# Kernel optimization log

Measured on AMD Instinct MI355X. Metric: run time of the kernel, lower is better.

## Reference

```python
import jax, jax.numpy as jnp
import numpy as np

HEADS = 8
DIM_HEAD = 64
SCALE = DIM_HEAD ** -0.5

B, N, DIM = 4096, 16, 512  # (batch*spatial, frames, channels)
HIDDEN = HEADS * DIM_HEAD  # 512


def setup_inputs() -> dict:
    key = jax.random.key(0)
    k1, k2, k3 = jax.random.split(key, 3)
    x = jax.random.normal(k1, (B, N, DIM), dtype=jnp.float32)
    # torch Linear(dim, 3*hidden, bias=False) applied as x @ W^T; we store the
    # transposed weight directly so forward is x @ w_qkv.
    w_qkv = jax.random.normal(k2, (DIM, 3 * HIDDEN), dtype=jnp.float32) * (DIM ** -0.5)
    w_out = jax.random.normal(k3, (HIDDEN, DIM), dtype=jnp.float32) * (HIDDEN ** -0.5)
    return {"x": x, "w_qkv": w_qkv, "w_out": w_out}


def reference(x, w_qkv, w_out):
    # qkv projection and split
    qkv = x @ w_qkv                                   # [b, n, 3*hidden]
    q, k, v = jnp.split(qkv, 3, axis=-1)              # each [b, n, hidden]

    def to_heads(t):
        b, n, _ = t.shape
        return t.reshape(b, n, HEADS, DIM_HEAD).transpose(0, 2, 1, 3)  # [b, h, n, d]

    q, k, v = to_heads(q), to_heads(k), to_heads(v)

    # linear attention feature maps
    q = jax.nn.softmax(q, axis=-1) * SCALE            # softmax over d
    k = jax.nn.softmax(k, axis=-2)                    # softmax over n

    # context = k^T v : [b, h, d, e]
    context = jnp.einsum('bhnd,bhne->bhde', k, v)
    out = jnp.einsum('bhnd,bhde->bhne', q, context)   # [b, h, n, e]

    b = out.shape[0]
    out = out.transpose(0, 2, 1, 3).reshape(b, N, HIDDEN)  # [b, n, hidden]
    return out @ w_out
```

## Files before the change

kernel.cpp:

```cpp
#include <hip/hip_runtime.h>
#include <hip/hip_bf16.h>


typedef __attribute__((ext_vector_type(8))) short bf16x8;
typedef __attribute__((ext_vector_type(4))) float f32x4;

__device__ __forceinline__ unsigned short f2bf(float f) {
  __hip_bfloat16 h = __float2bfloat16(f);
  return __builtin_bit_cast(unsigned short, h);
}
__device__ __forceinline__ float bf2f(unsigned short u) {
  unsigned int v = ((unsigned int)u) << 16;
  return __builtin_bit_cast(float, v);
}
__device__ __forceinline__ void gload16(const void* g, void* l) {
  __builtin_amdgcn_global_load_lds(
      (__attribute__((address_space(1))) void*)g,
      (__attribute__((address_space(3))) void*)l, 16, 0, 0);
}

__global__ __launch_bounds__(256) void conv_x_k(const float* __restrict__ x,
                                                unsigned short* __restrict__ xb) {
  size_t i = ((size_t)blockIdx.x * 256 + threadIdx.x) * 8;
  float4 a = *(const float4*)(x + i);
  float4 b = *(const float4*)(x + i + 4);
  union { unsigned short u[8]; bf16x8 v; } o;
  o.u[0] = f2bf(a.x); o.u[1] = f2bf(a.y); o.u[2] = f2bf(a.z); o.u[3] = f2bf(a.w);
  o.u[4] = f2bf(b.x); o.u[5] = f2bf(b.y); o.u[6] = f2bf(b.z); o.u[7] = f2bf(b.w);
  *(bf16x8*)(xb + i) = o.v;
}

__global__ __launch_bounds__(256) void conv_w_k(const float* __restrict__ wq,
                                                const float* __restrict__ wo,
                                                unsigned short* __restrict__ wqt,
                                                unsigned short* __restrict__ wot) {
  int i = blockIdx.x * 256 + threadIdx.x;
  if (i < 786432) {
    int n = i >> 9, k = i & 511;
    wqt[i] = f2bf(wq[k * 1536 + n]);
  } else {
    int j = i - 786432;
    int n = j >> 9, k = j & 511;
    wot[j] = f2bf(wo[k * 512 + n]);
  }
}

#define ABUF0 0
#define ABUF1 16384
#define BBUF0 32768
#define BBUF1 49152

__device__ __forceinline__ void stage_half(const unsigned short* __restrict__ G,
                                           int grow0, unsigned short* ldsb,
                                           int tid, int kofs) {
  int r = tid >> 3;
  int c = ((tid & 7) ^ (r & 7)) << 3;
  gload16(G + (size_t)(grow0 + r) * 512 + kofs + c, ldsb + tid * 8);
  gload16(G + (size_t)(grow0 + 64 + r) * 512 + kofs + c, ldsb + 4096 + tid * 8);
}

#define RD_A(base, mh, sw)                                                   \
  _Pragma("unroll") for (int mf = 0; mf < 4; ++mf)                           \
      aF[mf] = *(const bf16x8*)&lds[(base) + (rowA + (mh)*64 + mf*16) * 64 + (sw)];
#define RD_B(base, sw)                                                       \
  _Pragma("unroll") for (int nf = 0; nf < 4; ++nf)                           \
      bF[nf] = *(const bf16x8*)&lds[(base) + (rowB + nf*16) * 64 + (sw)];
#define DO_MFMA(mh)                                                          \
  __builtin_amdgcn_s_setprio(1);                                             \
  _Pragma("unroll") for (int mf = 0; mf < 4; ++mf)                           \
  _Pragma("unroll") for (int nf = 0; nf < 4; ++nf)                           \
      acc[(mh)*4 + mf][nf] = __builtin_amdgcn_mfma_f32_16x16x32_bf16(        \
          aF[mf], bF[nf], acc[(mh)*4 + mf][nf], 0, 0, 0);                    \
  __builtin_amdgcn_s_setprio(0);
#define PBAR() __builtin_amdgcn_s_barrier()
#define LGKM0()                                          \
  do {                                                   \
    asm volatile("s_waitcnt lgkmcnt(0)" ::: "memory");   \
    __builtin_amdgcn_sched_barrier(0);                   \
  } while (0)
#define VM2() asm volatile("s_waitcnt vmcnt(2)" ::: "memory")

template <int NTN, bool OUTBF>
__global__ __launch_bounds__(512) void gemm8_k(const unsigned short* __restrict__ A,
                                               const unsigned short* __restrict__ B,
                                               void* __restrict__ Cv) {
  __shared__ __align__(16) unsigned short lds[65536];
  int orig = blockIdx.x;
  int id = (orig & 7) * (gridDim.x >> 3) + (orig >> 3);
  int mt = id / NTN, nt = id % NTN;
  int m0 = mt * 256, n0 = nt * 256;
  int tid = threadIdx.x, wid = tid >> 6, l = tid & 63;
  int wr = wid >> 2, wc = wid & 3;
  int rowA = wr * 128 + (l & 15);
  int rowB = wc * 64 + (l & 15);
  int r7 = l & 7;
  int sw0 = ((l >> 4) ^ r7) << 3;
  int sw1 = (((l >> 4) | 4) ^ r7) << 3;

  f32x4 acc[8][4];
#pragma unroll
  for (int i = 0; i < 8; ++i)
#pragma unroll
    for (int j = 0; j < 4; ++j) acc[i][j] = (f32x4){0.f, 0.f, 0.f, 0.f};
  bf16x8 aF[4], bF[4];

  stage_half(B, n0,       lds + BBUF0,        tid, 0);
  stage_half(B, n0 + 128, lds + BBUF0 + 8192, tid, 0);
  stage_half(A, m0,       lds + ABUF0,        tid, 0);
  stage_half(A, m0 + 128, lds + ABUF0 + 8192, tid, 0);
  stage_half(B, n0,       lds + BBUF1,        tid, 64);
  VM2();
  PBAR();

  for (int it = 0; it < 4; ++it) {
    int k1 = (2 * it + 1) * 64;
    int t2 = 2 * it + 2; if (t2 > 7) t2 = 7;
    int t3 = 2 * it + 3; if (t3 > 7) t3 = 7;
    int k2 = t2 * 64, k3 = t3 * 64;

    RD_A(ABUF0, 0, sw0); RD_B(BBUF0, sw0);
    stage_half(B, n0 + 128, lds + BBUF1 + 8192, tid, k1);
    PBAR(); LGKM0(); DO_MFMA(0); PBAR();
    RD_A(ABUF0, 1, sw0);
    stage_half(A, m0, lds + ABUF1, tid, k1);
    PBAR(); LGKM0(); DO_MFMA(1); PBAR();
    RD_A(ABUF0, 0, sw1); RD_B(BBUF0, sw1);
    stage_half(A, m0 + 128, lds + ABUF1 + 8192, tid, k1);
    PBAR(); LGKM0(); DO_MFMA(0); PBAR();
    RD_A(ABUF0, 1, sw1);
    stage_half(B, n0, lds + BBUF0, tid, k2);
    VM2();
    PBAR(); LGKM0(); DO_MFMA(1); PBAR();
    RD_A(ABUF1, 0, sw0); RD_B(BBUF1, sw0);
    stage_half(B, n0 + 128, lds + BBUF0 + 8192, tid, k2);
    PBAR(); LGKM0(); DO_MFMA(0); PBAR();
    RD_A(ABUF1, 1, sw0);
    stage_half(A, m0, lds + ABUF0, tid, k2);
    PBAR(); LGKM0(); DO_MFMA(1); PBAR();
    RD_A(ABUF1, 0, sw1); RD_B(BBUF1, sw1);
    stage_half(A, m0 + 128, lds + ABUF0 + 8192, tid, k2);
    PBAR(); LGKM0(); DO_MFMA(0); PBAR();
    RD_A(ABUF1, 1, sw1);
    stage_half(B, n0, lds + BBUF1, tid, k3);
    VM2();
    PBAR(); LGKM0(); DO_MFMA(1); PBAR();
  }

#pragma unroll
  for (int m = 0; m < 8; ++m)
#pragma unroll
    for (int nf = 0; nf < 4; ++nf)
#pragma unroll
      for (int r = 0; r < 4; ++r) {
        int row = m0 + wr * 128 + m * 16 + (l >> 4) * 4 + r;
        int col = n0 + wc * 64 + nf * 16 + (l & 15);
        if (OUTBF)
          ((unsigned short*)Cv)[(size_t)row * (NTN * 256) + col] = f2bf(acc[m][nf][r]);
        else
          ((float*)Cv)[(size_t)row * (NTN * 256) + col] = acc[m][nf][r];
      }
}

#define QOFF 0
#define KOFF 1152
#define VOFF 2304
#define SOFF 3328
__global__ __launch_bounds__(256) void attn_k(const unsigned short* __restrict__ qkv,
                                              unsigned short* __restrict__ attn) {
  __shared__ __align__(16) unsigned short lds[4 * 3584];
  int tid = threadIdx.x, wid = tid >> 6, l = tid & 63;
  int p = blockIdx.x * 4 + wid;
  int b = p >> 3, h = p & 7;
  unsigned short* W = &lds[wid * 3584];
  const size_t rowb = (size_t)(b * 16) * 1536;

  float kv[16];
#pragma unroll
  for (int n = 0; n < 16; ++n) kv[n] = bf2f(qkv[rowb + n * 1536 + 512 + h * 64 + l]);
  float km = kv[0];
#pragma unroll
  for (int n = 1; n < 16; ++n) km = fmaxf(km, kv[n]);
  float ks = 0.f;
#pragma unroll
  for (int n = 0; n < 16; ++n) { kv[n] = __expf(kv[n] - km); ks += kv[n]; }
  float kinv = 1.f / ks;
#pragma unroll
  for (int n = 0; n < 16; ++n) W[KOFF + n * 72 + l] = f2bf(kv[n] * kinv);

#pragma unroll
  for (int n = 0; n < 16; ++n) {
    float x = bf2f(qkv[rowb + n * 1536 + h * 64 + l]);
    float mx = x;
    mx = fmaxf(mx, __shfl_xor(mx, 1));  mx = fmaxf(mx, __shfl_xor(mx, 2));
    mx = fmaxf(mx, __shfl_xor(mx, 4));  mx = fmaxf(mx, __shfl_xor(mx, 8));
    mx = fmaxf(mx, __shfl_xor(mx, 16)); mx = fmaxf(mx, __shfl_xor(mx, 32));
    float e = __expf(x - mx);
    float s = e;
    s += __shfl_xor(s, 1);  s += __shfl_xor(s, 2);  s += __shfl_xor(s, 4);
    s += __shfl_xor(s, 8);  s += __shfl_xor(s, 16); s += __shfl_xor(s, 32);
    W[QOFF + n * 72 + l] = f2bf(e / s * 0.125f);
  }

  const unsigned short* vp = qkv + rowb + (size_t)(l >> 2) * 1536 + 1024 + h * 64 + (l & 3) * 16;
  bf16x8 v0 = *(const bf16x8*)vp;
  bf16x8 v1 = *(const bf16x8*)(vp + 8);
#pragma unroll
  for (int c = 0; c < 8; ++c)
    W[VOFF + ((l & 3) * 16 + c) * 16 + (l >> 2)] = (unsigned short)v0[c];
#pragma unroll
  for (int c = 0; c < 8; ++c)
    W[VOFF + ((l & 3) * 16 + 8 + c) * 16 + (l >> 2)] = (unsigned short)v1[c];
  __syncthreads();

  f32x4 sacc = {0.f, 0.f, 0.f, 0.f};
#pragma unroll
  for (int kb = 0; kb < 2; ++kb) {
    bf16x8 a  = *(const bf16x8*)&W[QOFF + (l & 15) * 72 + kb * 32 + (l >> 4) * 8];
    bf16x8 bb = *(const bf16x8*)&W[KOFF + (l & 15) * 72 + kb * 32 + (l >> 4) * 8];
    sacc = __builtin_amdgcn_mfma_f32_16x16x32_bf16(a, bb, sacc, 0, 0, 0);
  }
#pragma unroll
  for (int r = 0; r < 4; ++r)
    W[SOFF + ((l >> 4) * 4 + r) * 16 + (l & 15)] = f2bf(sacc[r]);
  __syncthreads();

  bf16x8 zz = {0, 0, 0, 0, 0, 0, 0, 0};
  bf16x8 sa = zz;
  if (l < 32) sa = *(const bf16x8*)&W[SOFF + (l & 15) * 16 + (l >> 4) * 8];
#pragma unroll
  for (int et = 0; et < 4; ++et) {
    bf16x8 vb = zz;
    if (l < 32) vb = *(const bf16x8*)&W[VOFF + (et * 16 + (l & 15)) * 16 + (l >> 4) * 8];
    f32x4 o = {0.f, 0.f, 0.f, 0.f};
    o = __builtin_amdgcn_mfma_f32_16x16x32_bf16(sa, vb, o, 0, 0, 0);
#pragma unroll
    for (int r = 0; r < 4; ++r)
      attn[(size_t)(b * 16 + (l >> 4) * 4 + r) * 512 + h * 64 + et * 16 + (l & 15)] = f2bf(o[r]);
  }
}

extern "C" void kernel_launch(void* const* d_in, const int* in_sizes, int n_in,
                              void* d_out, int out_size, void* d_ws, size_t ws_size,
                              hipStream_t stream) {
  const float* x  = (const float*)d_in[0];
  const float* wq = (const float*)d_in[1];
  const float* wo = (const float*)d_in[2];
  float* out = (float*)d_out;

  unsigned short* xb   = (unsigned short*)d_ws;
  unsigned short* wqt  = xb  + 33554432;
  unsigned short* wot  = wqt + 786432;
  unsigned short* qkv  = wot + 262144;
  unsigned short* attn = xb;

  conv_x_k<<<16384, 256, 0, stream>>>(x, xb);
  conv_w_k<<<4096,  256, 0, stream>>>(wq, wo, wqt, wot);
  gemm8_k<6, true><<<1536, 512, 0, stream>>>(xb, wqt, qkv);
  attn_k<<<8192, 256, 0, stream>>>(qkv, attn);
  gemm8_k<2, false><<<512, 512, 0, stream>>>(attn, wot, out);
}
```

Measured before the change: 512.3 us.

## Restructure GEMM load pipeline and vectorize epilogue stores via swapped MFMA operands

```diff
diff --git a/kernel.cpp b/kernel.cpp
--- a/kernel.cpp
+++ b/kernel.cpp
@@ -70,15 +70,10 @@
   _Pragma("unroll") for (int mf = 0; mf < 4; ++mf)                           \
   _Pragma("unroll") for (int nf = 0; nf < 4; ++nf)                           \
       acc[(mh)*4 + mf][nf] = __builtin_amdgcn_mfma_f32_16x16x32_bf16(        \
-          aF[mf], bF[nf], acc[(mh)*4 + mf][nf], 0, 0, 0);                    \
+          bF[nf], aF[mf], acc[(mh)*4 + mf][nf], 0, 0, 0);                    \
   __builtin_amdgcn_s_setprio(0);
 #define PBAR() __builtin_amdgcn_s_barrier()
-#define LGKM0()                                          \
-  do {                                                   \
-    asm volatile("s_waitcnt lgkmcnt(0)" ::: "memory");   \
-    __builtin_amdgcn_sched_barrier(0);                   \
-  } while (0)
-#define VM2() asm volatile("s_waitcnt vmcnt(2)" ::: "memory")
+#define VM4() asm volatile("s_waitcnt vmcnt(4)" ::: "memory")
 
 template <int NTN, bool OUTBF>
 __global__ __launch_bounds__(512) void gemm8_k(const unsigned short* __restrict__ A,
@@ -109,7 +104,8 @@
   stage_half(A, m0,       lds + ABUF0,        tid, 0);
   stage_half(A, m0 + 128, lds + ABUF0 + 8192, tid, 0);
   stage_half(B, n0,       lds + BBUF1,        tid, 64);
-  VM2();
+  stage_half(B, n0 + 128, lds + BBUF1 + 8192, tid, 64);
+  VM4();
   PBAR();
 
   for (int it = 0; it < 4; ++it) {
@@ -119,46 +115,48 @@
     int k2 = t2 * 64, k3 = t3 * 64;
 
     RD_A(ABUF0, 0, sw0); RD_B(BBUF0, sw0);
-    stage_half(B, n0 + 128, lds + BBUF1 + 8192, tid, k1);
-    PBAR(); LGKM0(); DO_MFMA(0); PBAR();
+    stage_half(A, m0, lds + ABUF1, tid, k1);
+    PBAR(); DO_MFMA(0); PBAR();
     RD_A(ABUF0, 1, sw0);
-    stage_half(A, m0, lds + ABUF1, tid, k1);
-    PBAR(); LGKM0(); DO_MFMA(1); PBAR();
+    stage_half(A, m0 + 128, lds + ABUF1 + 8192, tid, k1);
+    PBAR(); DO_MFMA(1); PBAR();
     RD_A(ABUF0, 0, sw1); RD_B(BBUF0, sw1);
-    stage_half(A, m0 + 128, lds + ABUF1 + 8192, tid, k1);
-    PBAR(); LGKM0(); DO_MFMA(0); PBAR();
+    PBAR(); DO_MFMA(0); PBAR();
     RD_A(ABUF0, 1, sw1);
-    stage_half(B, n0, lds + BBUF0, tid, k2);
-    VM2();
-    PBAR(); LGKM0(); DO_MFMA(1); PBAR();
+    stage_half(B, n0,       lds + BBUF0,        tid, k2);
+    stage_half(B, n0 + 128, lds + BBUF0 + 8192, tid, k2);
+    PBAR(); DO_MFMA(1); VM4(); PBAR();
     RD_A(ABUF1, 0, sw0); RD_B(BBUF1, sw0);
-    stage_half(B, n0 + 128, lds + BBUF0 + 8192, tid, k2);
-    PBAR(); LGKM0(); DO_MFMA(0); PBAR();
+    stage_half(A, m0, lds + ABUF0, tid, k2);
+    PBAR(); DO_MFMA(0); PBAR();
     RD_A(ABUF1, 1, sw0);
-    stage_half(A, m0, lds + ABUF0, tid, k2);
-    PBAR(); LGKM0(); DO_MFMA(1); PBAR();
+    stage_half(A, m0 + 128, lds + ABUF0 + 8192, tid, k2);
+    PBAR(); DO_MFMA(1); PBAR();
     RD_A(ABUF1, 0, sw1); RD_B(BBUF1, sw1);
-    stage_half(A, m0 + 128, lds + ABUF0 + 8192, tid, k2);
-    PBAR(); LGKM0(); DO_MFMA(0); PBAR();
+    PBAR(); DO_MFMA(0); PBAR();
     RD_A(ABUF1, 1, sw1);
-    stage_half(B, n0, lds + BBUF1, tid, k3);
-    VM2();
-    PBAR(); LGKM0(); DO_MFMA(1); PBAR();
+    stage_half(B, n0,       lds + BBUF1,        tid, k3);
+    stage_half(B, n0 + 128, lds + BBUF1 + 8192, tid, k3);
+    PBAR(); DO_MFMA(1); VM4(); PBAR();
   }
 
 #pragma unroll
   for (int m = 0; m < 8; ++m)
 #pragma unroll
-    for (int nf = 0; nf < 4; ++nf)
-#pragma unroll
-      for (int r = 0; r < 4; ++r) {
-        int row = m0 + wr * 128 + m * 16 + (l >> 4) * 4 + r;
-        int col = n0 + wc * 64 + nf * 16 + (l & 15);
-        if (OUTBF)
-          ((unsigned short*)Cv)[(size_t)row * (NTN * 256) + col] = f2bf(acc[m][nf][r]);
-        else
-          ((float*)Cv)[(size_t)row * (NTN * 256) + col] = acc[m][nf][r];
+    for (int n = 0; n < 4; ++n) {
+      int row = m0 + wr * 128 + m * 16 + (l & 15);
+      int col = n0 + wc * 64 + n * 16 + (l >> 4) * 4;
+      if (OUTBF) {
+        unsigned int lo = (unsigned int)f2bf(acc[m][n][0]) |
+                          ((unsigned int)f2bf(acc[m][n][1]) << 16);
+        unsigned int hi = (unsigned int)f2bf(acc[m][n][2]) |
+                          ((unsigned int)f2bf(acc[m][n][3]) << 16);
+        uint2 pk = {lo, hi};
+        *(uint2*)((unsigned short*)Cv + (size_t)row * (NTN * 256) + col) = pk;
+      } else {
+        *(f32x4*)((float*)Cv + (size_t)row * (NTN * 256) + col) = acc[m][n];
       }
+    }
 }
 
 #define QOFF 0
```

Result: no change. 507.3 us (-1.0%).
